# Optimization experiments

Measured on AMD Instinct MI355X. Metric: run time of the kernel, lower is better.

## Reference

```python
import jax, jax.numpy as jnp
import numpy as np

B, S, D_IN, D_K, D_V = 4, 2048, 1024, 1024, 1024

def setup_inputs() -> dict:
    key = jax.random.key(0)
    ks = jax.random.split(key, 9)
    s = 0.02
    return {
        "query": jax.random.normal(ks[0], (B, S, D_IN), jnp.float32),
        "key_in": jax.random.normal(ks[1], (B, S, D_IN), jnp.float32),
        "value": jax.random.normal(ks[2], (B, S, D_IN), jnp.float32),
        "Wq": jax.random.normal(ks[3], (D_K, D_IN), jnp.float32) * s,
        "bq": jnp.zeros((D_K,), jnp.float32),
        "Wk": jax.random.normal(ks[4], (D_K, D_IN), jnp.float32) * s,
        "bk": jnp.zeros((D_K,), jnp.float32),
        "Wv": jax.random.normal(ks[5], (D_V, D_IN), jnp.float32) * s,
        "bv": jnp.zeros((D_V,), jnp.float32),
    }

def reference(query, key_in, value, Wq, bq, Wk, bk, Wv, bv):
    scale = D_K ** -0.5
    q = query @ Wq.T + bq          # [B,S,Dk]
    k = key_in @ Wk.T + bk         # [B,S,Dk]
    # Original quirk: self.v(value) is computed in __init__ but the forward
    # multiplies attn by the RAW value tensor, so Wv/bv are unused in the math.
    dots = jnp.einsum('bqd,bkd->bqk', q, k) * scale  # [B,S,S]
    attn = jax.nn.softmax(dots, axis=-1)
    out = jnp.einsum('bqk,bkd->bqd', attn, value)    # [B,S,D_IN]
    return out
```

## Files before the change

kernel.cpp:

```cpp
#include <hip/hip_runtime.h>
#include <hip/hip_bf16.h>
#include <stdint.h>

#define B_ 4
#define S_ 2048
#define D_ 1024

typedef __attribute__((ext_vector_type(8))) short short8;
typedef __attribute__((ext_vector_type(4))) float floatx4;

__device__ __forceinline__ unsigned short bf16_rne(float f) {
  union { float f; uint32_t u; } c; c.f = f;
  uint32_t u = c.u;
  return (unsigned short)((u + 0x7fffu + ((u >> 16) & 1u)) >> 16);
}

__device__ __forceinline__ void gl2lds16(const void* g, void* l) {
  __builtin_amdgcn_global_load_lds(
      (const __attribute__((address_space(1))) void*)g,
      (__attribute__((address_space(3))) void*)l, 16, 0, 0);
}

__global__ __launch_bounds__(256) void prep_all(
    const float* __restrict__ q, const float* __restrict__ k,
    const float* __restrict__ wq, const float* __restrict__ wk,
    const float* __restrict__ bq, const float* __restrict__ bk,
    const float* __restrict__ v,
    unsigned short* __restrict__ oq, unsigned short* __restrict__ ok,
    unsigned short* __restrict__ owq, unsigned short* __restrict__ owk,
    float* __restrict__ bias, unsigned short* __restrict__ vt) {
  __shared__ float tile[32][33];
  const int blk = blockIdx.x;
  if (blk < 18432) {
    int i = blk * 256 + threadIdx.x;
    const float* src; unsigned short* dst; int off;
    if (i < 2097152)      { src = q;  dst = oq;  off = i; }
    else if (i < 4194304) { src = k;  dst = ok;  off = i - 2097152; }
    else if (i < 4456448) { src = wq; dst = owq; off = i - 4194304; }
    else                  { src = wk; dst = owk; off = i - 4456448; }
    float4 vv = ((const float4*)src)[off];
    uint32_t p0 = (uint32_t)bf16_rne(vv.x) | ((uint32_t)bf16_rne(vv.y) << 16);
    uint32_t p1 = (uint32_t)bf16_rne(vv.z) | ((uint32_t)bf16_rne(vv.w) << 16);
    ((uint2*)dst)[off] = make_uint2(p0, p1);
  } else if (blk < 18434) {
    int j = (blk - 18432) * 256 + threadIdx.x;
    const float* src = (j < 256) ? bq : bk;
    ((float4*)bias)[j] = ((const float4*)src)[j & 255];
  } else {
    const int bi = blk - 18434;
    const int d0 = (bi & 31) * 32;
    const int s0 = ((bi >> 5) & 63) * 32;
    const int b  = bi >> 11;
    const int tx = threadIdx.x & 31, ty = threadIdx.x >> 5;
    const float* src = v + (size_t)b * S_ * D_;
#pragma unroll
    for (int i = 0; i < 4; ++i)
      tile[ty + i * 8][tx] = src[(size_t)(s0 + ty + i * 8) * D_ + d0 + tx];
    __syncthreads();
    unsigned short* dst = vt + (size_t)b * D_ * S_;
#pragma unroll
    for (int i = 0; i < 4; ++i)
      dst[(size_t)(d0 + ty + i * 8) * S_ + s0 + tx] = bf16_rne(tile[tx][ty + i * 8]);
  }
}

template <int EPI, int BM>
__global__ __launch_bounds__(256, BM == 128 ? 3 : 2) void gemm_bt(
    const unsigned short* __restrict__ A, const unsigned short* __restrict__ Bm,
    void* __restrict__ Cv, const float* __restrict__ bias,
    int N, int K, float scale,
    long long sA, long long sB, long long sC, long long sBias) {
  constexpr int IC = BM / 32;
  constexpr int AST = BM / 64;
  __shared__ unsigned short smA[2][BM * 32];
  __shared__ unsigned short smB[2][128 * 32];

  const int z = blockIdx.z;
  const unsigned short* Ab = A + (size_t)z * sA;
  const unsigned short* Bb = Bm + (size_t)z * sB;

  const int tile_n = blockIdx.x * 128;
  const int tile_m = blockIdx.y * BM;

  const int t = threadIdx.x;
  const int w = t >> 6;
  const int l = t & 63;
  const int wr = w >> 1, wc = w & 1;

  floatx4 acc[IC][4];
#pragma unroll
  for (int i = 0; i < IC; ++i)
#pragma unroll
    for (int j = 0; j < 4; ++j) acc[i][j] = (floatx4){0.f, 0.f, 0.f, 0.f};

  const int srow = l >> 2;
  const int scb = (l & 3) * 16;
  const int kc = (l >> 4) * 8;
  const int rm = l & 15;

  for (int kt = 0; kt < K; kt += 64) {
#pragma unroll
    for (int h = 0; h < 2; ++h) {
#pragma unroll
      for (int i = 0; i < AST; ++i) {
        const int r = (i * 4 + w) * 16 + srow;
        gl2lds16((const char*)Ab + ((size_t)(tile_m + r) * K + kt + h * 32) * 2 + scb,
                 (char*)smA[h] + (i * 4 + w) * 1024);
      }
#pragma unroll
      for (int i = 0; i < 2; ++i) {
        const int r = (i * 4 + w) * 16 + srow;
        gl2lds16((const char*)Bb + ((size_t)(tile_n + r) * K + kt + h * 32) * 2 + scb,
                 (char*)smB[h] + (i * 4 + w) * 1024);
      }
    }
    __syncthreads();

#pragma unroll
    for (int h = 0; h < 2; ++h) {
      short8 bfr[4];
#pragma unroll
      for (int j = 0; j < 4; ++j)
        bfr[j] = *(const short8*)(smB[h] + ((wc * 64 + j * 16 + rm) * 32 + kc));
#pragma unroll
      for (int i = 0; i < IC; ++i) {
        const short8 af = *(const short8*)(smA[h] + ((wr * (BM / 2) + i * 16 + rm) * 32 + kc));
#pragma unroll
        for (int j = 0; j < 4; ++j)
          acc[i][j] = __builtin_amdgcn_mfma_f32_16x16x32_bf16(af, bfr[j], acc[i][j], 0, 0, 0);
      }
    }
    __syncthreads();
  }

#pragma unroll
  for (int i = 0; i < IC; ++i) {
#pragma unroll
    for (int j = 0; j < 4; ++j) {
      const int n = tile_n + wc * 64 + j * 16 + rm;
      const int m0 = tile_m + wr * (BM / 2) + i * 16 + (l >> 4) * 4;
      if (EPI == 0) {
        const float bv = bias[(size_t)z * sBias + n];
        unsigned short* C = (unsigned short*)Cv + (size_t)z * sC;
#pragma unroll
        for (int r = 0; r < 4; ++r)
          C[(size_t)(m0 + r) * N + n] = bf16_rne(acc[i][j][r] + bv);
      } else if (EPI == 1) {
        float* C = (float*)Cv + (size_t)z * sC;
#pragma unroll
        for (int r = 0; r < 4; ++r)
          C[(size_t)(m0 + r) * N + n] = acc[i][j][r] * scale;
      } else {
        unsigned short* C = (unsigned short*)Cv + (size_t)z * sC;
#pragma unroll
        for (int r = 0; r < 4; ++r)
          C[(size_t)(m0 + r) * N + n] = bf16_rne(acc[i][j][r] * scale);
      }
    }
  }
}

__global__ __launch_bounds__(256) void softmax_bf16(
    const unsigned short* __restrict__ logits, unsigned short* __restrict__ attn) {
  const int row = blockIdx.x;
  const int t = threadIdx.x;
  uint4 raw = *(const uint4*)(logits + (size_t)row * S_ + t * 8);
  float x[8];
  const uint32_t ru[4] = {raw.x, raw.y, raw.z, raw.w};
#pragma unroll
  for (int i = 0; i < 4; ++i) {
    union { uint32_t u; float f; } lo, hi;
    lo.u = ru[i] << 16;
    hi.u = ru[i] & 0xffff0000u;
    x[2 * i] = lo.f;
    x[2 * i + 1] = hi.f;
  }
  float m = x[0];
#pragma unroll
  for (int i = 1; i < 8; ++i) m = fmaxf(m, x[i]);
#pragma unroll
  for (int off = 32; off > 0; off >>= 1) m = fmaxf(m, __shfl_xor(m, off));
  __shared__ float sm4[4], ss4[4];
  const int wv = t >> 6, ln = t & 63;
  if (ln == 0) sm4[wv] = m;
  __syncthreads();
  m = fmaxf(fmaxf(sm4[0], sm4[1]), fmaxf(sm4[2], sm4[3]));
  float s = 0.f;
  const float LOG2E = 1.44269504088896340736f;
#pragma unroll
  for (int i = 0; i < 8; ++i) {
    x[i] = exp2f((x[i] - m) * LOG2E);
    s += x[i];
  }
#pragma unroll
  for (int off = 32; off > 0; off >>= 1) s += __shfl_xor(s, off);
  if (ln == 0) ss4[wv] = s;
  __syncthreads();
  s = ss4[0] + ss4[1] + ss4[2] + ss4[3];
  const float inv = 1.0f / s;
  uint32_t p[4];
#pragma unroll
  for (int i = 0; i < 4; ++i)
    p[i] = (uint32_t)bf16_rne(x[2 * i] * inv) |
           ((uint32_t)bf16_rne(x[2 * i + 1] * inv) << 16);
  *(uint4*)(attn + (size_t)row * S_ + t * 8) = make_uint4(p[0], p[1], p[2], p[3]);
}

extern "C" void kernel_launch(void* const* d_in, const int* in_sizes, int n_in,
                              void* d_out, int out_size, void* d_ws, size_t ws_size,
                              hipStream_t stream) {
  (void)in_sizes; (void)n_in; (void)out_size; (void)ws_size;
  const float* query  = (const float*)d_in[0];
  const float* key_in = (const float*)d_in[1];
  const float* value  = (const float*)d_in[2];
  const float* Wq     = (const float*)d_in[3];
  const float* bq     = (const float*)d_in[4];
  const float* Wk     = (const float*)d_in[5];
  const float* bk     = (const float*)d_in[6];
  float* out = (float*)d_out;

  char* ws = (char*)d_ws;
  const size_t MiB = 1024 * 1024;
  unsigned short* Xq  = (unsigned short*)(ws);
  unsigned short* Xk  = (unsigned short*)(ws + 16 * MiB);
  unsigned short* Wqb = (unsigned short*)(ws + 32 * MiB);
  unsigned short* Wkb = (unsigned short*)(ws + 34 * MiB);
  float*          Bias= (float*)(ws + 36 * MiB);
  unsigned short* Vt  = (unsigned short*)(ws + 37 * MiB);
  unsigned short* Qp  = (unsigned short*)(ws + 53 * MiB);
  unsigned short* Kp  = (unsigned short*)(ws + 69 * MiB);
  unsigned short* Lg  = (unsigned short*)(ws + 85 * MiB);
  unsigned short* At  = (unsigned short*)(ws + 117 * MiB);

  prep_all<<<26626, 256, 0, stream>>>(query, key_in, Wq, Wk, bq, bk, value,
                                      Xq, Xk, Wqb, Wkb, Bias, Vt);

  gemm_bt<0, 256><<<dim3(D_ / 128, B_ * S_ / 256, 2), 256, 0, stream>>>(
      Xq, Wqb, Qp, Bias, D_, D_, 0.f,
      (long long)B_ * S_ * D_, (long long)D_ * D_, (long long)B_ * S_ * D_, D_);

  gemm_bt<2, 256><<<dim3(S_ / 128, S_ / 256, B_), 256, 0, stream>>>(
      Qp, Kp, Lg, nullptr, S_, D_, 0.03125f,
      (long long)S_ * D_, (long long)S_ * D_, (long long)S_ * S_, 0);

  softmax_bf16<<<B_ * S_, 256, 0, stream>>>(Lg, At);

  gemm_bt<1, 128><<<dim3(D_ / 128, S_ / 128, B_), 256, 0, stream>>>(
      At, Vt, out, nullptr, D_, S_, 1.0f,
      (long long)S_ * S_, (long long)D_ * S_, (long long)S_ * D_, 0);
}
```

Before: 304.6 us.

## Pipeline GEMM LDS loads across K steps with XOR-swizzled shared layout

The GEMM main loop now runs one 32-wide K slice per iteration with a two-stage ping-pong. The global-to-LDS load for the next slice is issued before the MFMAs run on the previous one, so memory latency can overlap compute. The LDS layout is XOR-swizzled on both the store and the fragment read to reduce bank conflicts. Occupancy hints are unified to 2 waves per SIMD. The diff leaves the __syncthreads placement out of view, so correctness depends on barriers being kept between the ping-pong stages.

```diff
diff --git a/kernel.cpp b/kernel.cpp
--- a/kernel.cpp
+++ b/kernel.cpp
@@ -65,7 +65,7 @@
 }
 
 template <int EPI, int BM>
-__global__ __launch_bounds__(256, BM == 128 ? 3 : 2) void gemm_bt(
+__global__ __launch_bounds__(256, 2) void gemm_bt(
     const unsigned short* __restrict__ A, const unsigned short* __restrict__ Bm,
     void* __restrict__ Cv, const float* __restrict__ bias,
     int N, int K, float scale,
@@ -94,37 +94,37 @@
     for (int j = 0; j < 4; ++j) acc[i][j] = (floatx4){0.f, 0.f, 0.f, 0.f};
 
   const int srow = l >> 2;
-  const int scb = (l & 3) * 16;
-  const int kc = (l >> 4) * 8;
-  const int rm = l & 15;
-
-  for (int kt = 0; kt < K; kt += 64) {
-#pragma unroll
-    for (int h = 0; h < 2; ++h) {
+  const int scb  = ((l & 3) ^ ((l >> 3) & 3)) * 16;
+  const int rm   = l & 15;
+  const int kcsw = ((l >> 4) ^ ((rm >> 1) & 3)) * 16;
+
+  for (int it = 0; it <= K >> 5; ++it) {
+    if (it < (K >> 5)) {
+      const int p = it & 1;
+      const int kb = it << 6;
 #pragma unroll
       for (int i = 0; i < AST; ++i) {
         const int r = (i * 4 + w) * 16 + srow;
-        gl2lds16((const char*)Ab + ((size_t)(tile_m + r) * K + kt + h * 32) * 2 + scb,
-                 (char*)smA[h] + (i * 4 + w) * 1024);
+        gl2lds16((const char*)Ab + (size_t)(tile_m + r) * K * 2 + kb + scb,
+                 (char*)smA[p] + (i * 4 + w) * 1024);
       }
 #pragma unroll
       for (int i = 0; i < 2; ++i) {
         const int r = (i * 4 + w) * 16 + srow;
-        gl2lds16((const char*)Bb + ((size_t)(tile_n + r) * K + kt + h * 32) * 2 + scb,
-                 (char*)smB[h] + (i * 4 + w) * 1024);
+        gl2lds16((const char*)Bb + (size_t)(tile_n + r) * K * 2 + kb + scb,
+                 (char*)smB[p] + (i * 4 + w) * 1024);
       }
     }
-    __syncthreads();
-
-#pragma unroll
-    for (int h = 0; h < 2; ++h) {
+    if (it > 0) {
+      const int p = (it - 1) & 1;
       short8 bfr[4];
 #pragma unroll
       for (int j = 0; j < 4; ++j)
-        bfr[j] = *(const short8*)(smB[h] + ((wc * 64 + j * 16 + rm) * 32 + kc));
+        bfr[j] = *(const short8*)((const char*)smB[p] + (wc * 64 + j * 16 + rm) * 64 + kcsw);
 #pragma unroll
       for (int i = 0; i < IC; ++i) {
-        const short8 af = *(const short8*)(smA[h] + ((wr * (BM / 2) + i * 16 + rm) * 32 + kc));
+        const short8 af = *(const short8*)((const char*)smA[p] +
+                                           (wr * (BM / 2) + i * 16 + rm) * 64 + kcsw);
 #pragma unroll
         for (int j = 0; j < 4; ++j)
           acc[i][j] = __builtin_amdgcn_mfma_f32_16x16x32_bf16(af, bfr[j], acc[i][j], 0, 0, 0);
```

Result: slower. 313.0 us (+2.7%).
